# Kernel optimization log

Hardware: AMD Instinct MI355X
Metric: run time of the kernel (lower is better)

The kernel has to match this reference:

```python
import jax, jax.numpy as jnp
import numpy as np

N_NODES, N_EDGES, D_IN, D_H, N_GRAPHS = 50000, 600000, 1024, 128, 1000


def _transformer_conv(x, src, dst, wq, bq, wk, bk, wv, bv, ws, bs, n):
    """PyG TransformerConv, heads=1, concat=True, root_weight=True."""
    q = x @ wq + bq                      # [N, d]
    k = x @ wk + bk
    v = x @ wv + bv
    d = q.shape[-1]
    # per-edge attention score for edge j->i: <q_i, k_j> / sqrt(d)
    score = jnp.sum(q[dst] * k[src], axis=-1) / jnp.sqrt(jnp.asarray(d, x.dtype))  # [E]
    # segment softmax over incoming edges of each destination node
    smax = jax.ops.segment_max(score, dst, num_segments=n)
    smax = jnp.where(jnp.isfinite(smax), smax, jnp.zeros_like(smax))
    ex = jnp.exp(score - smax[dst])
    denom = jax.ops.segment_sum(ex, dst, num_segments=n)
    alpha = ex / (denom[dst] + 1e-16)
    # scatter-aggregate weighted values back to destination nodes
    agg = jax.ops.segment_sum(alpha[:, None] * v[src], dst, num_segments=n)  # [N, d]
    # skip (root) connection
    return agg + x @ ws + bs


def setup_inputs() -> dict:
    key = jax.random.key(0)
    ks = jax.random.split(key, 20)
    inp = {}
    inp['x'] = jax.random.normal(ks[0], (N_NODES, D_IN), dtype=jnp.float32)
    inp['edge_index'] = jax.random.randint(ks[1], (2, N_EDGES), 0, N_NODES, dtype=jnp.int64)
    inp['idx'] = jax.random.randint(ks[2], (N_GRAPHS,), 0, N_NODES, dtype=jnp.int64)
    s_in = 0.02
    # layer 0: 1024 -> 128
    for i, nm in enumerate(['wq0', 'wk0', 'wv0', 'ws0']):
        inp[nm] = jax.random.normal(ks[3 + i], (D_IN, D_H), dtype=jnp.float32) * s_in
    for nm in ['bq0', 'bk0', 'bv0', 'bs0']:
        inp[nm] = jnp.zeros((D_H,), dtype=jnp.float32)
    # layer 1: 128 -> 128
    for i, nm in enumerate(['wq1', 'wk1', 'wv1', 'ws1']):
        inp[nm] = jax.random.normal(ks[7 + i], (D_H, D_H), dtype=jnp.float32) * 0.08
    for nm in ['bq1', 'bk1', 'bv1', 'bs1']:
        inp[nm] = jnp.zeros((D_H,), dtype=jnp.float32)
    # MLP head 128 -> 128 -> 64 -> 1
    inp['mw1'] = jax.random.normal(ks[11], (D_H, D_H), dtype=jnp.float32) * 0.08
    inp['mb1'] = jnp.zeros((D_H,), dtype=jnp.float32)
    inp['mw2'] = jax.random.normal(ks[12], (D_H, 64), dtype=jnp.float32) * 0.08
    inp['mb2'] = jnp.zeros((64,), dtype=jnp.float32)
    inp['mw3'] = jax.random.normal(ks[13], (64, 1), dtype=jnp.float32) * 0.1
    inp['mb3'] = jnp.zeros((1,), dtype=jnp.float32)
    return inp


def reference(x, edge_index, idx,
              wq0, bq0, wk0, bk0, wv0, bv0, ws0, bs0,
              wq1, bq1, wk1, bk1, wv1, bv1, ws1, bs1,
              mw1, mb1, mw2, mb2, mw3, mb3):
    src, dst = edge_index[0], edge_index[1]
    n = x.shape[0]
    h = _transformer_conv(x, src, dst, wq0, bq0, wk0, bk0, wv0, bv0, ws0, bs0, n)
    h = jax.nn.relu(h)
    h = _transformer_conv(h, src, dst, wq1, bq1, wk1, bk1, wv1, bv1, ws1, bs1, n)
    h = jax.nn.relu(h)
    h = h[idx]                           # one center node per graph -> [B, d]
    h = jax.nn.relu(h @ mw1 + mb1)       # dropout is identity in eval
    h = jax.nn.relu(h @ mw2 + mb2)
    out = jax.nn.sigmoid(h @ mw3 + mb3)  # [B, 1]
    return out
```

## Files before the change

### kernel.cpp

```cpp
#include <hip/hip_runtime.h>
#include <hip/hip_bf16.h>
#include <cstdint>
#include <cstddef>

typedef __bf16 bf16x2 __attribute__((ext_vector_type(2)));
typedef __bf16 bf16x8 __attribute__((ext_vector_type(8)));
typedef float f32x4 __attribute__((ext_vector_type(4)));

__device__ __forceinline__ void gl_lds16(const __bf16* g, __bf16* l) {
    __builtin_amdgcn_global_load_lds(
        (const __attribute__((address_space(1))) unsigned int*)g,
        (__attribute__((address_space(3))) unsigned int*)l, 16, 0, 0);
}

__global__ __launch_bounds__(256) void mark_idx_kernel(const int* __restrict__ idx,
                                                       int* __restrict__ flagIdx,
                                                       int* __restrict__ flagU, int B) {
    int t = blockIdx.x * 256 + threadIdx.x;
    if (t < B) {
        int n = idx[t];
        flagIdx[n] = 1;
        flagU[n] = 1;
    }
}

__global__ __launch_bounds__(256) void hist_mark_kernel(const int* __restrict__ esrc,
                                                        const int* __restrict__ edst,
                                                        const int* __restrict__ flagIdx,
                                                        int* __restrict__ deg,
                                                        int* __restrict__ flagU, int E) {
    int e = blockIdx.x * 256 + threadIdx.x;
    if (e < E) {
        int d = edst[e];
        atomicAdd(&deg[d], 1);
        if (flagIdx[d]) flagU[esrc[e]] = 1;
    }
}

__global__ __launch_bounds__(256) void compact_kernel(const int* __restrict__ flagU,
                                                      int* __restrict__ U,
                                                      int* __restrict__ nU, int N) {
    int i = blockIdx.x * 256 + threadIdx.x;
    if (i < N && flagU[i]) U[atomicAdd(nU, 1)] = i;
}

__global__ __launch_bounds__(1024) void scan8_kernel(const int* __restrict__ deg,
                                                     int* __restrict__ off, int n) {
    __shared__ int wsum[16];
    int tid = threadIdx.x, lane = tid & 63, wid = tid >> 6;
    if (tid == 0) off[0] = 0;
    int carry = 0;
    int nchunk = (n + 8191) >> 13;
    for (int c = 0; c < nchunk; ++c) {
        int base = (c << 13) + tid * 8;
        int4 a = *(const int4*)(deg + base);
        int4 b = *(const int4*)(deg + base + 4);
        int s[8];
        s[0] = a.x; s[1] = s[0] + a.y; s[2] = s[1] + a.z; s[3] = s[2] + a.w;
        s[4] = s[3] + b.x; s[5] = s[4] + b.y; s[6] = s[5] + b.z; s[7] = s[6] + b.w;
        int x = s[7];
        for (int o = 1; o < 64; o <<= 1) {
            int t = __shfl_up(x, o, 64);
            if (lane >= o) x += t;
        }
        if (lane == 63) wsum[wid] = x;
        __syncthreads();
        if (wid == 0 && lane < 16) {
            int w = wsum[lane];
            for (int o = 1; o < 16; o <<= 1) {
                int t = __shfl_up(w, o, 64);
                if (lane >= o) w += t;
            }
            wsum[lane] = w;
        }
        __syncthreads();
        int pre = carry + (wid ? wsum[wid - 1] : 0) + (x - s[7]);
#pragma unroll
        for (int i = 0; i < 8; ++i)
            if (base + i < n) off[base + i + 1] = pre + s[i];
        carry += wsum[15];
        __syncthreads();
    }
}

__global__ __launch_bounds__(256) void scatter_kernel(const int* __restrict__ src,
                                                      const int* __restrict__ dst,
                                                      const int* __restrict__ off,
                                                      int* __restrict__ cursor,
                                                      int* __restrict__ srcs, int E) {
    int e = blockIdx.x * 256 + threadIdx.x;
    if (e < E) {
        int d = dst[e];
        int p = off[d] + atomicAdd(&cursor[d], 1);
        srcs[p] = src[e];
    }
}

__global__ __launch_bounds__(256) void cast_bf16_kernel(const float* __restrict__ in,
                                                        __bf16* __restrict__ out, int n8) {
    int i = blockIdx.x * 256 + threadIdx.x;
    if (i >= n8) return;
    const float4* p = (const float4*)(in + (size_t)i * 8);
    float4 a = p[0], b = p[1];
    bf16x8 o = {(__bf16)a.x, (__bf16)a.y, (__bf16)a.z, (__bf16)a.w,
                (__bf16)b.x, (__bf16)b.y, (__bf16)b.z, (__bf16)b.w};
    *(bf16x8*)(out + (size_t)i * 8) = o;
}

__global__ __launch_bounds__(256) void pack_w_kernel(const float* __restrict__ wq0, const float* __restrict__ wk0,
                                                     const float* __restrict__ wv0, const float* __restrict__ ws0,
                                                     const float* __restrict__ wq1, const float* __restrict__ wk1,
                                                     const float* __restrict__ wv1, const float* __restrict__ ws1,
                                                     const float* __restrict__ bq0, const float* __restrict__ bk0,
                                                     const float* __restrict__ bv0, const float* __restrict__ bs0,
                                                     const float* __restrict__ bq1, const float* __restrict__ bk1,
                                                     const float* __restrict__ bv1, const float* __restrict__ bs1,
                                                     __bf16* __restrict__ w0t, __bf16* __restrict__ w1t,
                                                     float* __restrict__ b0, float* __restrict__ b1) {
    int i = blockIdx.x * 256 + threadIdx.x;
    const int S0 = 512 * 1024, S1 = 512 * 128;
    if (i < S0) {
        int n = i >> 10, k = i & 1023;
        int sel = n >> 7, c = n & 127;
        const float* w = (sel == 0) ? wk0 : (sel == 1) ? wv0 : (sel == 2) ? wq0 : ws0;
        w0t[i] = (__bf16)w[(size_t)k * 128 + c];
    } else if (i < S0 + S1) {
        int j = i - S0;
        int n = j >> 7, k = j & 127;
        int sel = n >> 7, c = n & 127;
        const float* w = (sel == 0) ? wk1 : (sel == 1) ? wv1 : (sel == 2) ? wq1 : ws1;
        w1t[j] = (__bf16)w[(size_t)k * 128 + c];
    } else if (i < S0 + S1 + 512) {
        int t = i - S0 - S1;
        int sel = t >> 7, c = t & 127;
        const float* b = (sel == 0) ? bk0 : (sel == 1) ? bv0 : (sel == 2) ? bq0 : bs0;
        b0[t] = b[c];
    } else if (i < S0 + S1 + 1024) {
        int t = i - S0 - S1 - 512;
        int sel = t >> 7, c = t & 127;
        const float* b = (sel == 0) ? bk1 : (sel == 1) ? bv1 : (sel == 2) ? bq1 : bs1;
        b1[t] = b[c];
    }
}

__global__ __launch_bounds__(256) void gemm_dual_kernel(const __bf16* __restrict__ A,
                                                        const __bf16* __restrict__ Bt,
                                                        const float* __restrict__ bias,
                                                        __bf16* __restrict__ outb,
                                                        float* __restrict__ outf,
                                                        const int* __restrict__ rl0,
                                                        const int* __restrict__ np0, int ns0,
                                                        const int* __restrict__ rl1,
                                                        const int* __restrict__ np1, int ns1,
                                                        int K) {
    __shared__ __align__(16) __bf16 Asl[128 * 32];
    __shared__ __align__(16) __bf16 Bsl[128 * 32];
    const int sector = blockIdx.x >> 1;
    const int nbase = (blockIdx.x & 1) << 7;
    const int* rowlist = sector ? rl1 : rl0;
    const int* nptr = sector ? np1 : np0;
    const int nrows = nptr ? *nptr : (sector ? ns1 : ns0);
    if (nrows <= 0) return;
    const __bf16* BT = Bt + (size_t)(sector ? 256 : 0) * K;
    const float* bs = bias + (sector ? 256 : 0);
    const int ntiles = (nrows + 127) >> 7;

    const int tid = threadIdx.x;
    const int lane = tid & 63, wid = tid >> 6;
    const int wm = wid >> 1, wn = wid & 1;
    const int fr = lane & 15, quad = lane >> 4;
    const int r0 = (wid << 4) + (lane >> 2);
    const int kc8 = (lane & 3) << 3;

    const __bf16* gB0 = BT + (size_t)(nbase + r0) * K + kc8;
    const __bf16* gB1 = BT + (size_t)(nbase + 64 + r0) * K + kc8;
    __bf16* ldsA0 = Asl + (size_t)(wid << 4) * 32;
    __bf16* ldsA1 = Asl + (size_t)(64 + (wid << 4)) * 32;
    __bf16* ldsB0 = Bsl + (size_t)(wid << 4) * 32;
    __bf16* ldsB1 = Bsl + (size_t)(64 + (wid << 4)) * 32;

    for (int mt = blockIdx.y; mt < ntiles; mt += gridDim.y) {
        const int mbase = mt << 7;
        int lr0 = mbase + r0;        if (lr0 >= nrows) lr0 = nrows - 1;
        int lr1 = mbase + 64 + r0;   if (lr1 >= nrows) lr1 = nrows - 1;
        const int gr0 = rowlist ? rowlist[lr0] : lr0;
        const int gr1 = rowlist ? rowlist[lr1] : lr1;
        const __bf16* gA0 = A + (size_t)gr0 * K + kc8;
        const __bf16* gA1 = A + (size_t)gr1 * K + kc8;

        f32x4 acc[4][4];
#pragma unroll
        for (int i = 0; i < 4; i++)
#pragma unroll
            for (int j = 0; j < 4; j++) acc[i][j] = (f32x4){0.f, 0.f, 0.f, 0.f};

        for (int k0 = 0; k0 < K; k0 += 32) {
            __syncthreads();
            gl_lds16(gA0 + k0, ldsA0);
            gl_lds16(gA1 + k0, ldsA1);
            gl_lds16(gB0 + k0, ldsB0);
            gl_lds16(gB1 + k0, ldsB1);
            __syncthreads();
            bf16x8 af[4], bfr[4];
#pragma unroll
            for (int mi = 0; mi < 4; mi++)
                af[mi] = *(const bf16x8*)(Asl + (size_t)(wm * 64 + mi * 16 + fr) * 32 + quad * 8);
#pragma unroll
            for (int ni = 0; ni < 4; ni++)
                bfr[ni] = *(const bf16x8*)(Bsl + (size_t)(wn * 64 + ni * 16 + fr) * 32 + quad * 8);
#pragma unroll
            for (int mi = 0; mi < 4; mi++)
#pragma unroll
                for (int ni = 0; ni < 4; ni++)
                    acc[mi][ni] = __builtin_amdgcn_mfma_f32_16x16x32_bf16(af[mi], bfr[ni], acc[mi][ni], 0, 0, 0);
        }

#pragma unroll
        for (int mi = 0; mi < 4; mi++)
#pragma unroll
            for (int ni = 0; ni < 4; ni++) {
                int rl = wm * 64 + mi * 16 + quad * 4;
                int cl = wn * 64 + ni * 16 + fr;
                float b = bs[nbase + cl];
                int gcol = nbase + cl;
#pragma unroll
                for (int r = 0; r < 4; r++) {
                    int lr = mbase + rl + r;
                    if (lr < nrows) {
                        int gr = rowlist ? rowlist[lr] : lr;
                        float v = acc[mi][ni][r] + b;
                        if (sector == 0) outb[(size_t)gr * 256 + gcol] = (__bf16)v;
                        else             outf[(size_t)gr * 256 + gcol] = v;
                    }
                }
            }
        __syncthreads();
    }
}

__global__ __launch_bounds__(256) void attn_kernel(const float* __restrict__ qs,
                                                   const __bf16* __restrict__ kvb,
                                                   const int* __restrict__ off,
                                                   const int* __restrict__ srcs,
                                                   const int* __restrict__ nodelist,
                                                   const int* __restrict__ nptr, int nstatic,
                                                   __bf16* __restrict__ outb,
                                                   float* __restrict__ outf, int mode) {
    int n = nptr ? *nptr : nstatic;
    int lane = threadIdx.x & 63;
    int w0 = blockIdx.x * 4 + (threadIdx.x >> 6);
    int nw = gridDim.x * 4;
    const float scale = 0.08838834764831845f;
    for (int w = w0; w < n; w += nw) {
        int node = nodelist ? nodelist[w] : w;
        const float* bq = qs + (size_t)node * 256;
        float2 q = *(const float2*)(bq + 2 * lane);
        float2 s = *(const float2*)(bq + 128 + 2 * lane);
        int e0 = off[node], e1 = off[node + 1];
        float m = -INFINITY, l = 0.f;
        float ax = 0.f, ay = 0.f;
        bf16x2 kc = {(__bf16)0.f, (__bf16)0.f}, vc = kc;
        if (e0 < e1) {
            const __bf16* p = kvb + (size_t)srcs[e0] * 256;
            kc = *(const bf16x2*)(p + 2 * lane);
            vc = *(const bf16x2*)(p + 128 + 2 * lane);
        }
        for (int e = e0; e < e1; ++e) {
            bf16x2 kn = {(__bf16)0.f, (__bf16)0.f}, vn = kn;
            if (e + 1 < e1) {
                const __bf16* p = kvb + (size_t)srcs[e + 1] * 256;
                kn = *(const bf16x2*)(p + 2 * lane);
                vn = *(const bf16x2*)(p + 128 + 2 * lane);
            }
            float t = q.x * (float)kc.x + q.y * (float)kc.y;
#pragma unroll
            for (int o = 32; o > 0; o >>= 1) t += __shfl_xor(t, o, 64);
            float sc = t * scale;
            float mn = fmaxf(m, sc);
            float al = __expf(m - mn);
            float ee = __expf(sc - mn);
            ax = ax * al + ee * (float)vc.x;
            ay = ay * al + ee * (float)vc.y;
            l = l * al + ee;
            m = mn;
            kc = kn; vc = vn;
        }
        float inv = 1.f / (l + 1e-16f);
        float ox = ax * inv + s.x, oy = ay * inv + s.y;
        if (mode) {
            bf16x2 o2 = {(__bf16)fmaxf(ox, 0.f), (__bf16)fmaxf(oy, 0.f)};
            *(bf16x2*)(outb + (size_t)node * 128 + 2 * lane) = o2;
        } else {
            float2 o2 = {fmaxf(ox, 0.f), fmaxf(oy, 0.f)};
            *(float2*)(outf + (size_t)w * 128 + 2 * lane) = o2;
        }
    }
}

__global__ __launch_bounds__(128) void mlp_kernel(const float* __restrict__ hbuf,
                                                  const float* __restrict__ mw1, const float* __restrict__ mb1,
                                                  const float* __restrict__ mw2, const float* __restrict__ mb2,
                                                  const float* __restrict__ mw3, const float* __restrict__ mb3,
                                                  float* __restrict__ out, int B) {
    int b = blockIdx.x;
    int t = threadIdx.x;
    if (b >= B) return;
    __shared__ float xr[128], z1[128], z2[64];
    xr[t] = hbuf[(size_t)b * 128 + t];
    __syncthreads();
    float a1 = mb1[t];
#pragma unroll 8
    for (int k = 0; k < 128; ++k) a1 += xr[k] * mw1[k * 128 + t];
    z1[t] = fmaxf(a1, 0.f);
    __syncthreads();
    if (t < 64) {
        float a2 = mb2[t];
#pragma unroll 8
        for (int k = 0; k < 128; ++k) a2 += z1[k] * mw2[k * 64 + t];
        z2[t] = fmaxf(a2, 0.f);
    }
    __syncthreads();
    if (t < 64) {
        float p = z2[t] * mw3[t];
#pragma unroll
        for (int o = 32; o > 0; o >>= 1) p += __shfl_xor(p, o, 64);
        if (t == 0) out[b] = 1.f / (1.f + __expf(-(p + mb3[0])));
    }
}

extern "C" void kernel_launch(void* const* d_in, const int* in_sizes, int n_in,
                              void* d_out, int out_size, void* d_ws, size_t ws_size,
                              hipStream_t stream) {
    const float* x   = (const float*)d_in[0];
    const int*   ei  = (const int*)d_in[1];
    const int*   idx = (const int*)d_in[2];
    const float* wq0 = (const float*)d_in[3];
    const float* wk0 = (const float*)d_in[4];
    const float* wv0 = (const float*)d_in[5];
    const float* ws0 = (const float*)d_in[6];
    const float* bq0 = (const float*)d_in[7];
    const float* bk0 = (const float*)d_in[8];
    const float* bv0 = (const float*)d_in[9];
    const float* bs0 = (const float*)d_in[10];
    const float* wq1 = (const float*)d_in[11];
    const float* wk1 = (const float*)d_in[12];
    const float* wv1 = (const float*)d_in[13];
    const float* ws1 = (const float*)d_in[14];
    const float* bq1 = (const float*)d_in[15];
    const float* bk1 = (const float*)d_in[16];
    const float* bv1 = (const float*)d_in[17];
    const float* bs1 = (const float*)d_in[18];
    const float* mw1 = (const float*)d_in[19];
    const float* mb1 = (const float*)d_in[20];
    const float* mw2 = (const float*)d_in[21];
    const float* mb2 = (const float*)d_in[22];
    const float* mw3 = (const float*)d_in[23];
    const float* mb3 = (const float*)d_in[24];
    float* out = (float*)d_out;

    const int Nn = in_sizes[0] / 1024;
    const int E  = in_sizes[1] / 2;
    const int B  = in_sizes[2];
    const int* esrc = ei;
    const int* edst = ei + E;
    const int degPad = ((Nn + 8191) >> 13) << 13;

    uintptr_t base = (uintptr_t)d_ws;
    auto alloc = [&](size_t bytes) -> void* {
        uintptr_t p = (base + 255) & ~(uintptr_t)255;
        base = p + bytes;
        return (void*)p;
    };
    __bf16* xb   = (__bf16*)alloc((size_t)Nn * 1024 * 2);
    __bf16* h0b  = (__bf16*)xb;
    __bf16* kvb  = (__bf16*)alloc((size_t)Nn * 256 * 2);
    __bf16* kv1b = kvb;
    float*  qs   = (float*)alloc((size_t)Nn * 256 * 4);
    float*  qs1  = qs;
    float*  hbuf = (float*)alloc((size_t)B * 128 * 4);
    __bf16* w0t  = (__bf16*)alloc(512 * 1024 * 2);
    __bf16* w1t  = (__bf16*)alloc(512 * 128 * 2);
    float*  b0   = (float*)alloc(512 * 4);
    float*  b1   = (float*)alloc(512 * 4);
    int* deg     = (int*)alloc((size_t)degPad * 4);
    int* cursor  = (int*)alloc((size_t)Nn * 4);
    int* flagIdx = (int*)alloc((size_t)Nn * 4);
    int* flagU   = (int*)alloc((size_t)Nn * 4);
    int* nU      = (int*)alloc(256);
    size_t zbytes = (uintptr_t)nU + 256 - (uintptr_t)deg;
    int* off     = (int*)alloc((size_t)(Nn + 1) * 4);
    int* srcs    = (int*)alloc((size_t)E * 4);
    int* U       = (int*)alloc((size_t)Nn * 4);

    hipMemsetAsync(deg, 0, zbytes, stream);

    mark_idx_kernel<<<(B + 255) / 256, 256, 0, stream>>>(idx, flagIdx, flagU, B);
    hist_mark_kernel<<<(E + 255) / 256, 256, 0, stream>>>(esrc, edst, flagIdx, deg, flagU, E);
    scan8_kernel<<<1, 1024, 0, stream>>>(deg, off, Nn);
    scatter_kernel<<<(E + 255) / 256, 256, 0, stream>>>(esrc, edst, off, cursor, srcs, E);
    compact_kernel<<<(Nn + 255) / 256, 256, 0, stream>>>(flagU, U, nU, Nn);

    pack_w_kernel<<<(512 * 1024 + 512 * 128 + 1024 + 255) / 256, 256, 0, stream>>>(
        wq0, wk0, wv0, ws0, wq1, wk1, wv1, ws1,
        bq0, bk0, bv0, bs0, bq1, bk1, bv1, bs1, w0t, w1t, b0, b1);
    int n8 = Nn * 1024 / 8;
    cast_bf16_kernel<<<(n8 + 255) / 256, 256, 0, stream>>>(x, xb, n8);

    const int mtiles = (Nn + 127) / 128;

    gemm_dual_kernel<<<dim3(4, mtiles), 256, 0, stream>>>(xb, w0t, b0, kvb, qs,
                                                          nullptr, nullptr, Nn,
                                                          U, nU, 0, 1024);
    attn_kernel<<<4096, 256, 0, stream>>>(qs, kvb, off, srcs, U, nU, 0, h0b, nullptr, 1);

    gemm_dual_kernel<<<dim3(4, 96), 256, 0, stream>>>(h0b, w1t, b1, kv1b, qs1,
                                                      U, nU, 0,
                                                      idx, nullptr, B, 128);
    attn_kernel<<<(B + 3) / 4, 256, 0, stream>>>(qs1, kv1b, off, srcs, idx, nullptr, B, nullptr, hbuf, 0);

    mlp_kernel<<<B, 128, 0, stream>>>(hbuf, mw1, mb1, mw2, mb2, mw3, mb3, out, B);
}
```

Measured before the change: 641.6 us.

## Fuse fp32-to-bf16 cast into GEMM A-load and double-buffer LDS tiles

Removes the separate cast kernel that converted the 50000x1024 fp32 input to bf16. The first GEMM now reads fp32 directly, converts in registers and stores to LDS. The GEMM also gains a two-stage LDS double buffer, so the next K-slice is prefetched while MFMAs run on the current one, with one barrier per iteration instead of two. The costs are doubled LDS use, fp32 A reads that move twice the bytes per element through registers instead of the direct global-to-LDS path, and a separate h0b buffer.

Measured after the change: 681.6 us. +6.2%, slower.

```diff
diff --git a/kernel.cpp b/kernel.cpp
--- a/kernel.cpp
+++ b/kernel.cpp
@@ -11,6 +11,18 @@
     __builtin_amdgcn_global_load_lds(
         (const __attribute__((address_space(1))) unsigned int*)g,
         (__attribute__((address_space(3))) unsigned int*)l, 16, 0, 0);
+}
+
+template <typename AT>
+__device__ __forceinline__ bf16x8 loadA8(const AT* p) {
+    if constexpr (sizeof(AT) == 4) {
+        float4 u = *(const float4*)p;
+        float4 v = *(const float4*)(p + 4);
+        return (bf16x8){(__bf16)u.x, (__bf16)u.y, (__bf16)u.z, (__bf16)u.w,
+                        (__bf16)v.x, (__bf16)v.y, (__bf16)v.z, (__bf16)v.w};
+    } else {
+        return *(const bf16x8*)p;
+    }
 }
 
 __global__ __launch_bounds__(256) void mark_idx_kernel(const int* __restrict__ idx,
@@ -94,17 +106,6 @@
         int p = off[d] + atomicAdd(&cursor[d], 1);
         srcs[p] = src[e];
     }
-}
-
-__global__ __launch_bounds__(256) void cast_bf16_kernel(const float* __restrict__ in,
-                                                        __bf16* __restrict__ out, int n8) {
-    int i = blockIdx.x * 256 + threadIdx.x;
-    if (i >= n8) return;
-    const float4* p = (const float4*)(in + (size_t)i * 8);
-    float4 a = p[0], b = p[1];
-    bf16x8 o = {(__bf16)a.x, (__bf16)a.y, (__bf16)a.z, (__bf16)a.w,
-                (__bf16)b.x, (__bf16)b.y, (__bf16)b.z, (__bf16)b.w};
-    *(bf16x8*)(out + (size_t)i * 8) = o;
 }
 
 __global__ __launch_bounds__(256) void pack_w_kernel(const float* __restrict__ wq0, const float* __restrict__ wk0,
@@ -143,7 +144,8 @@
     }
 }
 
-__global__ __launch_bounds__(256) void gemm_dual_kernel(const __bf16* __restrict__ A,
+template <typename AT>
+__global__ __launch_bounds__(256) void gemm_dual_kernel(const AT* __restrict__ A,
                                                         const __bf16* __restrict__ Bt,
                                                         const float* __restrict__ bias,
                                                         __bf16* __restrict__ outb,
@@ -153,8 +155,8 @@
                                                         const int* __restrict__ rl1,
                                                         const int* __restrict__ np1, int ns1,
                                                         int K) {
-    __shared__ __align__(16) __bf16 Asl[128 * 32];
-    __shared__ __align__(16) __bf16 Bsl[128 * 32];
+    __shared__ __align__(16) __bf16 Asl[2][128 * 32];
+    __shared__ __align__(16) __bf16 Bsl[2][128 * 32];
     const int sector = blockIdx.x >> 1;
     const int nbase = (blockIdx.x & 1) << 7;
     const int* rowlist = sector ? rl1 : rl0;
@@ -164,29 +166,30 @@
     const __bf16* BT = Bt + (size_t)(sector ? 256 : 0) * K;
     const float* bs = bias + (sector ? 256 : 0);
     const int ntiles = (nrows + 127) >> 7;
+    const int nk = K >> 5;
 
     const int tid = threadIdx.x;
     const int lane = tid & 63, wid = tid >> 6;
     const int wm = wid >> 1, wn = wid & 1;
     const int fr = lane & 15, quad = lane >> 4;
-    const int r0 = (wid << 4) + (lane >> 2);
+    const int rr = (wid << 4) + (lane >> 2);
     const int kc8 = (lane & 3) << 3;
 
-    const __bf16* gB0 = BT + (size_t)(nbase + r0) * K + kc8;
-    const __bf16* gB1 = BT + (size_t)(nbase + 64 + r0) * K + kc8;
-    __bf16* ldsA0 = Asl + (size_t)(wid << 4) * 32;
-    __bf16* ldsA1 = Asl + (size_t)(64 + (wid << 4)) * 32;
-    __bf16* ldsB0 = Bsl + (size_t)(wid << 4) * 32;
-    __bf16* ldsB1 = Bsl + (size_t)(64 + (wid << 4)) * 32;
+    const __bf16* gB0 = BT + (size_t)(nbase + rr) * K + kc8;
+    const __bf16* gB1 = BT + (size_t)(nbase + 64 + rr) * K + kc8;
+    const int ldsBoff0 = (wid << 4) * 32;
+    const int ldsBoff1 = (64 + (wid << 4)) * 32;
+    const int ldsAoff0 = rr * 32 + kc8;
+    const int ldsAoff1 = (64 + rr) * 32 + kc8;
 
     for (int mt = blockIdx.y; mt < ntiles; mt += gridDim.y) {
         const int mbase = mt << 7;
-        int lr0 = mbase + r0;        if (lr0 >= nrows) lr0 = nrows - 1;
-        int lr1 = mbase + 64 + r0;   if (lr1 >= nrows) lr1 = nrows - 1;
+        int lr0 = mbase + rr;        if (lr0 >= nrows) lr0 = nrows - 1;
+        int lr1 = mbase + 64 + rr;   if (lr1 >= nrows) lr1 = nrows - 1;
         const int gr0 = rowlist ? rowlist[lr0] : lr0;
         const int gr1 = rowlist ? rowlist[lr1] : lr1;
-        const __bf16* gA0 = A + (size_t)gr0 * K + kc8;
-        const __bf16* gA1 = A + (size_t)gr1 * K + kc8;
+        const AT* gA0 = A + (size_t)gr0 * K + kc8;
+        const AT* gA1 = A + (size_t)gr1 * K + kc8;
 
         f32x4 acc[4][4];
 #pragma unroll
@@ -194,25 +197,44 @@
 #pragma unroll
             for (int j = 0; j < 4; j++) acc[i][j] = (f32x4){0.f, 0.f, 0.f, 0.f};
 
-        for (int k0 = 0; k0 < K; k0 += 32) {
-            __syncthreads();
-            gl_lds16(gA0 + k0, ldsA0);
-            gl_lds16(gA1 + k0, ldsA1);
-            gl_lds16(gB0 + k0, ldsB0);
-            gl_lds16(gB1 + k0, ldsB1);
-            __syncthreads();
+        gl_lds16(gB0, &Bsl[0][ldsBoff0]);
+        gl_lds16(gB1, &Bsl[0][ldsBoff1]);
+        {
+            bf16x8 p0 = loadA8(gA0);
+            bf16x8 p1 = loadA8(gA1);
+            *(bf16x8*)&Asl[0][ldsAoff0] = p0;
+            *(bf16x8*)&Asl[0][ldsAoff1] = p1;
+        }
+        __syncthreads();
+
+        for (int kk = 0; kk < nk; ++kk) {
+            const int p = kk & 1, q = p ^ 1;
+            const bool more = (kk + 1) < nk;
+            bf16x8 n0, n1;
+            if (more) {
+                const int ko = (kk + 1) << 5;
+                gl_lds16(gB0 + ko, &Bsl[q][ldsBoff0]);
+                gl_lds16(gB1 + ko, &Bsl[q][ldsBoff1]);
+                n0 = loadA8(gA0 + ko);
+                n1 = loadA8(gA1 + ko);
+            }
             bf16x8 af[4], bfr[4];
 #pragma unroll
             for (int mi = 0; mi < 4; mi++)
-                af[mi] = *(const bf16x8*)(Asl + (size_t)(wm * 64 + mi * 16 + fr) * 32 + quad * 8);
+                af[mi] = *(const bf16x8*)&Asl[p][(wm * 64 + mi * 16 + fr) * 32 + quad * 8];
 #pragma unroll
             for (int ni = 0; ni < 4; ni++)
-                bfr[ni] = *(const bf16x8*)(Bsl + (size_t)(wn * 64 + ni * 16 + fr) * 32 + quad * 8);
+                bfr[ni] = *(const bf16x8*)&Bsl[p][(wn * 64 + ni * 16 + fr) * 32 + quad * 8];
 #pragma unroll
             for (int mi = 0; mi < 4; mi++)
 #pragma unroll
                 for (int ni = 0; ni < 4; ni++)
                     acc[mi][ni] = __builtin_amdgcn_mfma_f32_16x16x32_bf16(af[mi], bfr[ni], acc[mi][ni], 0, 0, 0);
+            if (more) {
+                *(bf16x8*)&Asl[q][ldsAoff0] = n0;
+                *(bf16x8*)&Asl[q][ldsAoff1] = n1;
+            }
+            __syncthreads();
         }
 
 #pragma unroll
@@ -234,7 +256,6 @@
                     }
                 }
             }
-        __syncthreads();
     }
 }
 
@@ -371,12 +392,11 @@
         base = p + bytes;
         return (void*)p;
     };
-    __bf16* xb   = (__bf16*)alloc((size_t)Nn * 1024 * 2);
-    __bf16* h0b  = (__bf16*)xb;
     __bf16* kvb  = (__bf16*)alloc((size_t)Nn * 256 * 2);
     __bf16* kv1b = kvb;
     float*  qs   = (float*)alloc((size_t)Nn * 256 * 4);
     float*  qs1  = qs;
+    __bf16* h0b  = (__bf16*)alloc((size_t)Nn * 128 * 2);
     float*  hbuf = (float*)alloc((size_t)B * 128 * 4);
     __bf16* w0t  = (__bf16*)alloc(512 * 1024 * 2);
     __bf16* w1t  = (__bf16*)alloc(512 * 128 * 2);
@@ -403,19 +423,17 @@
     pack_w_kernel<<<(512 * 1024 + 512 * 128 + 1024 + 255) / 256, 256, 0, stream>>>(
         wq0, wk0, wv0, ws0, wq1, wk1, wv1, ws1,
         bq0, bk0, bv0, bs0, bq1, bk1, bv1, bs1, w0t, w1t, b0, b1);
-    int n8 = Nn * 1024 / 8;
-    cast_bf16_kernel<<<(n8 + 255) / 256, 256, 0, stream>>>(x, xb, n8);
 
     const int mtiles = (Nn + 127) / 128;
 
-    gemm_dual_kernel<<<dim3(4, mtiles), 256, 0, stream>>>(xb, w0t, b0, kvb, qs,
-                                                          nullptr, nullptr, Nn,
-                                                          U, nU, 0, 1024);
+    gemm_dual_kernel<float><<<dim3(4, mtiles), 256, 0, stream>>>(x, w0t, b0, kvb, qs,
+                                                                 nullptr, nullptr, Nn,
+                                                                 U, nU, 0, 1024);
     attn_kernel<<<4096, 256, 0, stream>>>(qs, kvb, off, srcs, U, nU, 0, h0b, nullptr, 1);
 
-    gemm_dual_kernel<<<dim3(4, 96), 256, 0, stream>>>(h0b, w1t, b1, kv1b, qs1,
-                                                      U, nU, 0,
-                                                      idx, nullptr, B, 128);
+    gemm_dual_kernel<__bf16><<<dim3(4, 96), 256, 0, stream>>>(h0b, w1t, b1, kv1b, qs1,
+                                                              U, nU, 0,
+                                                              idx, nullptr, B, 128);
     attn_kernel<<<(B + 3) / 4, 256, 0, stream>>>(qs1, kv1b, off, srcs, idx, nullptr, B, nullptr, hbuf, 0);
 
     mlp_kernel<<<B, 128, 0, stream>>>(hbuf, mw1, mb1, mw2, mb2, mw3, mb3, out, B);
```

## Fuse fp32-to-bf16 cast into GEMM A-load and fold compaction into scan

Applied to the files above, without the earlier changes.

The layer-0 GEMM now reads fp32 x directly and converts to bf16 in registers before writing to LDS. This removes the separate cast kernel and its full round trip of a 50000x1024 bf16 copy through memory. The GEMM block grows to 512 threads (8 waves, each computing 64x32) with a one-row-per-thread load mapping. The compact kernel is folded into the tail of the single-block scan kernel to save a launch. The trade-off is that A now goes through synchronous register loads instead of direct global-to-LDS transfers, and K-steps re-read fp32 data at twice the bytes. The compaction also now runs serially in one block.

New measurement: 639.6 us. Within noise of the previous version (-0.3%).

```diff
diff --git a/kernel.cpp b/kernel.cpp
--- a/kernel.cpp
+++ b/kernel.cpp
@@ -11,6 +11,18 @@
     __builtin_amdgcn_global_load_lds(
         (const __attribute__((address_space(1))) unsigned int*)g,
         (__attribute__((address_space(3))) unsigned int*)l, 16, 0, 0);
+}
+
+template <typename AT>
+__device__ __forceinline__ bf16x8 loadA8(const AT* p) {
+    if constexpr (sizeof(AT) == 4) {
+        float4 u = *(const float4*)p;
+        float4 v = *(const float4*)(p + 4);
+        return (bf16x8){(__bf16)u.x, (__bf16)u.y, (__bf16)u.z, (__bf16)u.w,
+                        (__bf16)v.x, (__bf16)v.y, (__bf16)v.z, (__bf16)v.w};
+    } else {
+        return *(const bf16x8*)p;
+    }
 }
 
 __global__ __launch_bounds__(256) void mark_idx_kernel(const int* __restrict__ idx,
@@ -37,15 +49,11 @@
     }
 }
 
-__global__ __launch_bounds__(256) void compact_kernel(const int* __restrict__ flagU,
-                                                      int* __restrict__ U,
-                                                      int* __restrict__ nU, int N) {
-    int i = blockIdx.x * 256 + threadIdx.x;
-    if (i < N && flagU[i]) U[atomicAdd(nU, 1)] = i;
-}
-
 __global__ __launch_bounds__(1024) void scan8_kernel(const int* __restrict__ deg,
-                                                     int* __restrict__ off, int n) {
+                                                     int* __restrict__ off, int n,
+                                                     const int* __restrict__ flagU,
+                                                     int* __restrict__ U,
+                                                     int* __restrict__ nU) {
     __shared__ int wsum[16];
     int tid = threadIdx.x, lane = tid & 63, wid = tid >> 6;
     if (tid == 0) off[0] = 0;
@@ -81,6 +89,8 @@
         carry += wsum[15];
         __syncthreads();
     }
+    for (int i = tid; i < n; i += 1024)
+        if (flagU[i]) U[atomicAdd(nU, 1)] = i;
 }
 
 __global__ __launch_bounds__(256) void scatter_kernel(const int* __restrict__ src,
@@ -94,17 +104,6 @@
         int p = off[d] + atomicAdd(&cursor[d], 1);
         srcs[p] = src[e];
     }
-}
-
-__global__ __launch_bounds__(256) void cast_bf16_kernel(const float* __restrict__ in,
-                                                        __bf16* __restrict__ out, int n8) {
-    int i = blockIdx.x * 256 + threadIdx.x;
-    if (i >= n8) return;
-    const float4* p = (const float4*)(in + (size_t)i * 8);
-    float4 a = p[0], b = p[1];
-    bf16x8 o = {(__bf16)a.x, (__bf16)a.y, (__bf16)a.z, (__bf16)a.w,
-                (__bf16)b.x, (__bf16)b.y, (__bf16)b.z, (__bf16)b.w};
-    *(bf16x8*)(out + (size_t)i * 8) = o;
 }
 
 __global__ __launch_bounds__(256) void pack_w_kernel(const float* __restrict__ wq0, const float* __restrict__ wk0,
@@ -143,7 +142,8 @@
     }
 }
 
-__global__ __launch_bounds__(256) void gemm_dual_kernel(const __bf16* __restrict__ A,
+template <typename AT>
+__global__ __launch_bounds__(512) void gemm_dual_kernel(const AT* __restrict__ A,
                                                         const __bf16* __restrict__ Bt,
                                                         const float* __restrict__ bias,
                                                         __bf16* __restrict__ outb,
@@ -167,70 +167,63 @@
 
     const int tid = threadIdx.x;
     const int lane = tid & 63, wid = tid >> 6;
-    const int wm = wid >> 1, wn = wid & 1;
+    const int wm = wid >> 2, wn = wid & 3;
     const int fr = lane & 15, quad = lane >> 4;
-    const int r0 = (wid << 4) + (lane >> 2);
-    const int kc8 = (lane & 3) << 3;
-
-    const __bf16* gB0 = BT + (size_t)(nbase + r0) * K + kc8;
-    const __bf16* gB1 = BT + (size_t)(nbase + 64 + r0) * K + kc8;
-    __bf16* ldsA0 = Asl + (size_t)(wid << 4) * 32;
-    __bf16* ldsA1 = Asl + (size_t)(64 + (wid << 4)) * 32;
-    __bf16* ldsB0 = Bsl + (size_t)(wid << 4) * 32;
-    __bf16* ldsB1 = Bsl + (size_t)(64 + (wid << 4)) * 32;
+    const int rr = tid >> 2;
+    const int kc8 = (tid & 3) << 3;
+
+    const __bf16* gB = BT + (size_t)(nbase + rr) * K + kc8;
+    __bf16* ldsB = Bsl + (size_t)(wid << 4) * 32;
 
     for (int mt = blockIdx.y; mt < ntiles; mt += gridDim.y) {
         const int mbase = mt << 7;
-        int lr0 = mbase + r0;        if (lr0 >= nrows) lr0 = nrows - 1;
-        int lr1 = mbase + 64 + r0;   if (lr1 >= nrows) lr1 = nrows - 1;
-        const int gr0 = rowlist ? rowlist[lr0] : lr0;
-        const int gr1 = rowlist ? rowlist[lr1] : lr1;
-        const __bf16* gA0 = A + (size_t)gr0 * K + kc8;
-        const __bf16* gA1 = A + (size_t)gr1 * K + kc8;
-
-        f32x4 acc[4][4];
+        int lr = mbase + rr;
+        if (lr >= nrows) lr = nrows - 1;
+        const int gr = rowlist ? rowlist[lr] : lr;
+        const AT* gA = A + (size_t)gr * K + kc8;
+
+        f32x4 acc[4][2];
 #pragma unroll
         for (int i = 0; i < 4; i++)
 #pragma unroll
-            for (int j = 0; j < 4; j++) acc[i][j] = (f32x4){0.f, 0.f, 0.f, 0.f};
+            for (int j = 0; j < 2; j++) acc[i][j] = (f32x4){0.f, 0.f, 0.f, 0.f};
 
         for (int k0 = 0; k0 < K; k0 += 32) {
             __syncthreads();
-            gl_lds16(gA0 + k0, ldsA0);
-            gl_lds16(gA1 + k0, ldsA1);
-            gl_lds16(gB0 + k0, ldsB0);
-            gl_lds16(gB1 + k0, ldsB1);
+            gl_lds16(gB + k0, ldsB);
+            bf16x8 a8 = loadA8(gA + k0);
+            *(bf16x8*)&Asl[rr * 32 + kc8] = a8;
             __syncthreads();
-            bf16x8 af[4], bfr[4];
+            bf16x8 af[4], bfr[2];
 #pragma unroll
             for (int mi = 0; mi < 4; mi++)
-                af[mi] = *(const bf16x8*)(Asl + (size_t)(wm * 64 + mi * 16 + fr) * 32 + quad * 8);
-#pragma unroll
-            for (int ni = 0; ni < 4; ni++)
-                bfr[ni] = *(const bf16x8*)(Bsl + (size_t)(wn * 64 + ni * 16 + fr) * 32 + quad * 8);
+                af[mi] = *(const bf16x8*)&Asl[(wm * 64 + mi * 16 + fr) * 32 + quad * 8];
+#pragma unroll
+            for (int ni = 0; ni < 2; ni++)
+                bfr[ni] = *(const bf16x8*)&Bsl[(wn * 32 + ni * 16 + fr) * 32 + quad * 8];
 #pragma unroll
             for (int mi = 0; mi < 4; mi++)
 #pragma unroll
-                for (int ni = 0; ni < 4; ni++)
+                for (int ni = 0; ni < 2; ni++)
                     acc[mi][ni] = __builtin_amdgcn_mfma_f32_16x16x32_bf16(af[mi], bfr[ni], acc[mi][ni], 0, 0, 0);
         }
 
 #pragma unroll
         for (int mi = 0; mi < 4; mi++)
 #pragma unroll
-            for (int ni = 0; ni < 4; ni++) {
+            for (int ni = 0; ni < 2; ni++) {
                 int rl = wm * 64 + mi * 16 + quad * 4;
-                int cl = wn * 64 + ni * 16 + fr;
+                int cl = wn * 32 + ni * 16 + fr;
                 float b = bs[nbase + cl];
                 int gcol = nbase + cl;
 #pragma unroll
                 for (int r = 0; r < 4; r++) {
-                    int lr = mbase + rl + r;
-                    if (lr < nrows) {
-                        int gr = rowlist ? rowlist[lr] : lr;
+                    int lr2 = mbase + rl + r;
+                    if (lr2 < nrows) {
+                        int gr2 = rowlist ? rowlist[lr2] : lr2;
                         float v = acc[mi][ni][r] + b;
-                        if (sector == 0) outb[(size_t)gr * 256 + gcol] = (__bf16)v;
-                        else             outf[(size_t)gr * 256 + gcol] = v;
+                        if (sector == 0) outb[(size_t)gr2 * 256 + gcol] = (__bf16)v;
+                        else             outf[(size_t)gr2 * 256 + gcol] = v;
                     }
                 }
             }
@@ -371,12 +364,11 @@
         base = p + bytes;
         return (void*)p;
     };
-    __bf16* xb   = (__bf16*)alloc((size_t)Nn * 1024 * 2);
-    __bf16* h0b  = (__bf16*)xb;
     __bf16* kvb  = (__bf16*)alloc((size_t)Nn * 256 * 2);
     __bf16* kv1b = kvb;
     float*  qs   = (float*)alloc((size_t)Nn * 256 * 4);
     float*  qs1  = qs;
+    __bf16* h0b  = (__bf16*)alloc((size_t)Nn * 128 * 2);
     float*  hbuf = (float*)alloc((size_t)B * 128 * 4);
     __bf16* w0t  = (__bf16*)alloc(512 * 1024 * 2);
     __bf16* w1t  = (__bf16*)alloc(512 * 128 * 2);
@@ -396,26 +388,23 @@
 
     mark_idx_kernel<<<(B + 255) / 256, 256, 0, stream>>>(idx, flagIdx, flagU, B);
     hist_mark_kernel<<<(E + 255) / 256, 256, 0, stream>>>(esrc, edst, flagIdx, deg, flagU, E);
-    scan8_kernel<<<1, 1024, 0, stream>>>(deg, off, Nn);
+    scan8_kernel<<<1, 1024, 0, stream>>>(deg, off, Nn, flagU, U, nU);
     scatter_kernel<<<(E + 255) / 256, 256, 0, stream>>>(esrc, edst, off, cursor, srcs, E);
-    compact_kernel<<<(Nn + 255) / 256, 256, 0, stream>>>(flagU, U, nU, Nn);
 
     pack_w_kernel<<<(512 * 1024 + 512 * 128 + 1024 + 255) / 256, 256, 0, stream>>>(
         wq0, wk0, wv0, ws0, wq1, wk1, wv1, ws1,
         bq0, bk0, bv0, bs0, bq1, bk1, bv1, bs1, w0t, w1t, b0, b1);
-    int n8 = Nn * 1024 / 8;
-    cast_bf16_kernel<<<(n8 + 255) / 256, 256, 0, stream>>>(x, xb, n8);
 
     const int mtiles = (Nn + 127) / 128;
 
-    gemm_dual_kernel<<<dim3(4, mtiles), 256, 0, stream>>>(xb, w0t, b0, kvb, qs,
-                                                          nullptr, nullptr, Nn,
-                                                          U, nU, 0, 1024);
+    gemm_dual_kernel<float><<<dim3(4, mtiles), 512, 0, stream>>>(x, w0t, b0, kvb, qs,
+                                                                 nullptr, nullptr, Nn,
+                                                                 U, nU, 0, 1024);
     attn_kernel<<<4096, 256, 0, stream>>>(qs, kvb, off, srcs, U, nU, 0, h0b, nullptr, 1);
 
-    gemm_dual_kernel<<<dim3(4, 96), 256, 0, stream>>>(h0b, w1t, b1, kv1b, qs1,
-                                                      U, nU, 0,
-                                                      idx, nullptr, B, 128);
+    gemm_dual_kernel<__bf16><<<dim3(4, 96), 512, 0, stream>>>(h0b, w1t, b1, kv1b, qs1,
+                                                              U, nU, 0,
+                                                              idx, nullptr, B, 128);
     attn_kernel<<<(B + 3) / 4, 256, 0, stream>>>(qs1, kv1b, off, srcs, idx, nullptr, B, nullptr, hbuf, 0);
 
     mlp_kernel<<<B, 128, 0, stream>>>(hbuf, mw1, mb1, mw2, mb2, mw3, mb3, out, B);
```
